# Kernel optimization log

Measured on AMD Instinct MI355X. Metric: run time of the kernel, lower is better.

Reference implementation:

```python
import jax, jax.numpy as jnp
import numpy as np
from jax import lax

B, D, H, W = 2, 96, 96, 96
K = 3          # static upper bound on connected components (setup builds exactly 3 blobs)
CC_ITERS = 48  # >= max component diameter under 26-connectivity label propagation
V = D * H * W
BIGI = jnp.int32(V)  # sentinel label for background


def _make_target():
    # 3 well-separated spherical lesions per volume -> exactly K connected components
    centers = [(20, 20, 20), (70, 30, 60), (40, 75, 75)]
    r2 = 9 ** 2
    zz, yy, xx = np.meshgrid(np.arange(D), np.arange(H), np.arange(W), indexing='ij')
    vol = np.zeros((D, H, W), np.float32)
    for cz, cy, cx in centers:
        vol[(zz - cz) ** 2 + (yy - cy) ** 2 + (xx - cx) ** 2 <= r2] = 1.0
    return jnp.asarray(np.stack([vol, np.roll(vol, 5, axis=2)])[:, None])  # [B,1,D,H,W]


def setup_inputs() -> dict:
    key = jax.random.key(0)
    pred = jax.random.normal(key, (B, 1, D, H, W), jnp.float32)
    return {"pred": pred, "target": _make_target()}


def _connected_components(mask):
    # 26-connectivity labeling (matches skimage/cucim default for 3D).
    # Label = min flat raster index in each component, so ascending-sorted labels
    # reproduce cucim's scan-order labels 1..N (needed for tie-breaking parity).
    lab = jnp.where(mask, jnp.arange(V, dtype=jnp.int32).reshape(mask.shape), BIGI)
    for _ in range(CC_ITERS):  # fixed unroll; components have diameter << CC_ITERS
        nb = lax.reduce_window(lab, BIGI, lax.min, (3, 3, 3), (1, 1, 1), 'SAME')
        lab = jnp.where(mask, nb, BIGI)
    return lab


def _edt1d(f):
    # exact 1D squared-distance lower envelope: d[i] = min_j f[j] + (i-j)^2
    n = f.shape[-1]
    i = jnp.arange(n, dtype=jnp.float32)
    sq = (i[:, None] - i[None, :]) ** 2  # [n_out, n_in]
    return jnp.min(f[..., None, :] + sq, axis=-1)


def _squared_edt(seed):
    # exact squared Euclidean distance-to-seed via 3 separable passes
    f = jnp.where(seed, jnp.float32(0), jnp.float32(1e12))
    for ax in range(3):
        f = jnp.moveaxis(_edt1d(jnp.moveaxis(f, ax, -1)), -1, ax)
    return f


def _forward(pred, target):
    p = jax.nn.sigmoid(pred)[:, 0]  # dim==5 -> sigmoid; squeeze channel -> [B,D,H,W]
    g = target[:, 0]

    def labels(gt):
        lab = _connected_components(gt > 0.5)
        ul = jnp.unique(lab, size=K + 1, fill_value=BIGI)[:K]  # ascending = scan order
        return lab, ul

    lab, ul = jax.vmap(labels)(g)                 # lab [B,D,H,W], ul [B,K]
    valid = (ul < BIGI).astype(p.dtype)           # [B,K]
    seeds = lab[:, None] == ul[:, :, None, None, None]  # [B,K,D,H,W] bool
    # serial map over (B*K) regions keeps the [D,H,W,n] EDT intermediate to one at a time
    dists = lax.map(_squared_edt, seeds.reshape(B * K, D, H, W)).reshape(B, K, D, H, W)
    # squared vs sqrt distance: same ordering AND same ties as torch's strict '<' update;
    rmap = jnp.argmin(dists, axis=1)              # Voronoi region map [B,D,H,W]

    oh = jax.nn.one_hot(rmap, K, dtype=p.dtype)   # [B,D,H,W,K]
    inter = jnp.einsum('bdhw,bdhwk->bk', p * g, oh)
    psum = jnp.einsum('bdhw,bdhwk->bk', p, oh)
    gsum = jnp.einsum('bdhw,bdhwk->bk', g, oh)
    dice = 2.0 * inter / (psum + gsum + 1e-8)
    cnt = jnp.sum(valid, axis=1)
    mean_dice = jnp.sum(dice * valid, axis=1) / jnp.maximum(cnt, 1.0)
    loss = jnp.where(cnt > 0, 1.0 - mean_dice, 1.0)  # num_features==0 -> loss 1.0
    return jnp.mean(loss)


def reference(pred, target):
    return _forward(pred, target)
```

## Files before the change

### kernel.cpp

```cpp
#include <hip/hip_runtime.h>
#include <math.h>

#define SLICE 9216
#define VOL 884736
#define NB 2
#define KK 3
#define BIGI VOL
#define BIGP 0x3FFFFFFC
#define BIGPF 1.0e9f
#define CC_SWEEPS 4
#define NYC 4
#define NZC 4
#define NPART (NB*96*NZC)
#define MAXROW 64
#define MAXNZ 64
#define YSTR (MAXNZ*96)

#define OFF_ACT   (NB*VOL*4)
#define OFF_DISTC (2*NB*VOL*4)
#define DISTC_BYTES (NB*96*MAXNZ*96*4)
#define OFF_SMALL (OFF_DISTC + DISTC_BYTES)
#define OFF_ZMASK (OFF_SMALL + 64)
#define OFF_ROOTS (OFF_SMALL + 128)
#define OFF_MASK  (OFF_SMALL + 1024)
#define MASK_ULL  (NB*KK*96*96*2)
#define OFF_PART  (OFF_MASK + MASK_ULL*8)
#define OFF_M8    (OFF_PART + NPART*9*4)

__global__ void k_init(const float4* __restrict__ tgt4, int* __restrict__ lab,
                       int* __restrict__ act, int* __restrict__ small,
                       unsigned long long* __restrict__ masks,
                       unsigned char* __restrict__ m8) {
  int q = blockIdx.x * 256 + threadIdx.x;
  if (q < MASK_ULL) masks[q] = 0;
  if (q >= NB * VOL / 4) return;
  float4 tv = tgt4[q];
  int base = q * 4;
  int bo = (base >= VOL) ? VOL : 0;
  int4 lv;
  lv.x = (tv.x > 0.5f) ? base - bo     : BIGI;
  lv.y = (tv.y > 0.5f) ? base - bo + 1 : BIGI;
  lv.z = (tv.z > 0.5f) ? base - bo + 2 : BIGI;
  lv.w = (tv.w > 0.5f) ? base - bo + 3 : BIGI;
  ((int4*)lab)[q] = lv;
  unsigned char mb = (tv.x > 0.5f ? 1 : 0) | (tv.y > 0.5f ? 2 : 0) |
                     (tv.z > 0.5f ? 4 : 0) | (tv.w > 0.5f ? 8 : 0);
  m8[q] = mb;
  int cnt = (lv.x != BIGI) + (lv.y != BIGI) + (lv.z != BIGI) + (lv.w != BIGI);
  if (cnt) {
    int pos = atomicAdd(&small[0], cnt);
    if (lv.x != BIGI) act[pos++] = base;
    if (lv.y != BIGI) act[pos++] = base + 1;
    if (lv.z != BIGI) act[pos++] = base + 2;
    if (lv.w != BIGI) act[pos]   = base + 3;
  }
}

__global__ void k_prop(int* __restrict__ lab, const int* __restrict__ act,
                       int* __restrict__ small, int record,
                       int* __restrict__ roots) {
  int n = small[0];
  for (int i = blockIdx.x * blockDim.x + threadIdx.x; i < n;
       i += gridDim.x * blockDim.x) {
    int idx = act[i];
    int bo = (idx >= VOL) ? VOL : 0;
    int v = idx - bo;
    int z = v / SLICE;
    int rem = v - z * SLICE;
    int y = rem / 96;
    int x = rem - y * 96;
    int* L = lab + bo;
    int z0 = z > 0 ? z - 1 : 0, z1 = z < 95 ? z + 1 : 95;
    int y0 = y > 0 ? y - 1 : 0, y1 = y < 95 ? y + 1 : 95;
    int x0 = x > 0 ? x - 1 : 0, x1 = x < 95 ? x + 1 : 95;
    int m = BIGI;
    for (int zz = z0; zz <= z1; zz++)
      for (int yy = y0; yy <= y1; yy++) {
        const int* row = L + zz * SLICE + yy * 96;
        for (int xx = x0; xx <= x1; xx++) m = min(m, row[xx]);
      }
    int m2 = L[m];
    int m3 = L[m2];
    int m4 = L[m3];
    lab[idx] = m4;
    if (record && m4 == v) {
      int b = bo ? 1 : 0;
      int pos = atomicAdd(&small[1 + b], 1);
      if (pos < 64) roots[b * 64 + pos] = v;
    }
  }
}

__global__ void k_seeds(const int* __restrict__ lab, const int* __restrict__ act,
                        const int* __restrict__ small, const int* __restrict__ roots,
                        unsigned long long* __restrict__ masks,
                        unsigned long long* __restrict__ zmg) {
  __shared__ int s_roots[128];
  __shared__ int s_ul[NB][KK];
  __shared__ unsigned long long zm[NB * 2];
  int t = threadIdx.x;
  if (t < 128) {
    int b = t >> 6, j = t & 63;
    int nr = small[1 + b]; if (nr > 64) nr = 64;
    s_roots[t] = (j < nr) ? roots[t] : 0x7fffffff;
  }
  if (t < NB * KK) s_ul[t / KK][t % KK] = -2;
  if (t < NB * 2) zm[t] = 0;
  __syncthreads();
  if (t < 128) {
    int r = s_roots[t];
    if (r != 0x7fffffff) {
      int b = t >> 6;
      int rank = 0;
      #pragma unroll
      for (int j = 0; j < 64; j++)
        rank += (s_roots[(b << 6) + j] < r) ? 1 : 0;
      if (rank < KK) s_ul[b][rank] = r;
    }
  }
  __syncthreads();
  int n = small[0];
  for (int i = blockIdx.x * 256 + t; i < n; i += gridDim.x * 256) {
    int idx = act[i];
    int b = (idx >= VOL) ? 1 : 0;
    int v = idx - (b ? VOL : 0);
    const int* L = lab + (b ? VOL : 0);
    int lv = L[v];
    int nx = L[lv];
    while (nx != lv) { lv = nx; nx = L[lv]; }
    int k = (lv == s_ul[b][0]) ? 0 : (lv == s_ul[b][1]) ? 1
          : (lv == s_ul[b][2]) ? 2 : -1;
    if (k >= 0) {
      int z = v / SLICE;
      int rem = v - z * SLICE;
      int y = rem / 96;
      int x = rem - y * 96;
      unsigned long long* M =
          masks + (((size_t)(b * KK + k) * 96 + z) * 96 + y) * 2;
      if (x < 64) atomicOr(&M[0], 1ull << x);
      else        atomicOr(&M[1], 1ull << (x - 64));
      if (z < 64) atomicOr(&zm[b * 2],     1ull << z);
      else        atomicOr(&zm[b * 2 + 1], 1ull << (z - 64));
    }
  }
  __syncthreads();
  if (t < NB * 2 && zm[t]) atomicOr(&zmg[t], zm[t]);
}

__device__ __forceinline__ int row_dist(unsigned long long lo,
                                        unsigned long long hi, int x) {
  int dr, dlft;
  {
    unsigned long long rl, rh;
    if (x == 0)      { rl = lo; rh = hi; }
    else if (x < 64) { rl = (lo >> x) | (hi << (64 - x)); rh = hi >> x; }
    else             { rl = hi >> (x - 64); rh = 0; }
    dr = rl ? (__ffsll(rl) - 1) : (rh ? (63 + __ffsll(rh)) : 1000);
  }
  {
    unsigned long long ll, lh;
    if (x >= 64) { ll = lo; lh = hi & ((2ull << (x - 64)) - 1); }
    else         { ll = lo & ((2ull << x) - 1); lh = 0; }
    dlft = lh ? (x - 127 + __clzll(lh))
              : (ll ? (x - 63 + __clzll(ll)) : 1000);
  }
  return min(dr, dlft);
}

__global__ __launch_bounds__(256) void k_edt_xy(const unsigned long long* __restrict__ masks,
                                                const unsigned long long* __restrict__ zmg,
                                                float* __restrict__ distC) {
  int blk = blockIdx.x;
  int b = blk / (MAXNZ * NYC);
  int rem = blk - b * MAXNZ * NYC;
  int jj = rem / NYC;
  int yc = rem - jj * NYC;
  unsigned long long zlo = zmg[b * 2], zhi = zmg[b * 2 + 1];
  int nlo = __popcll(zlo);
  int nz = nlo + __popcll(zhi);
  if (jj >= nz) return;
  int z;
  if (jj < nlo) {
    unsigned long long w = zlo;
    for (int i = 0; i < jj; i++) w &= w - 1;
    z = __ffsll(w) - 1;
  } else {
    unsigned long long w = zhi;
    int r2 = jj - nlo;
    for (int i = 0; i < r2; i++) w &= w - 1;
    z = 64 + __ffsll(w) - 1;
  }
  __shared__ unsigned long long sM[KK * 192];
  __shared__ float pl[MAXROW * 96];
  __shared__ unsigned char vrow[96];
  __shared__ int s_n;
  int t = threadIdx.x;
  if (t == 0) s_n = 0;
  for (int i = t; i < KK * 192; i += 256) {
    int k = i / 192, r = i - k * 192;
    sM[i] = masks[((size_t)(b * KK + k) * 96 + z) * 192 + r];
  }
  __syncthreads();
  if (t < 96) {
    unsigned long long any = sM[t * 2] | sM[t * 2 + 1] | sM[192 + t * 2] |
                             sM[193 + t * 2] | sM[384 + t * 2] | sM[385 + t * 2];
    if (any) {
      int pos = atomicAdd(&s_n, 1);
      if (pos < MAXROW) vrow[pos] = (unsigned char)t;
    }
  }
  __syncthreads();
  int n = s_n; if (n > MAXROW) n = MAXROW;
  for (int i = t; i < n * 96; i += 256) {
    int j2 = i / 96, x = i - j2 * 96;
    int y = vrow[j2];
    int best = BIGP;
    #pragma unroll
    for (int k = 0; k < KK; k++) {
      unsigned long long lo = sM[k * 192 + y * 2];
      unsigned long long hi = sM[k * 192 + y * 2 + 1];
      if (lo | hi) {
        int d = row_dist(lo, hi, x);
        best = min(best, ((d * d) << 2) | k);
      }
    }
    pl[j2 * 96 + x] = (best == BIGP) ? BIGPF : (float)best;
  }
  __syncthreads();
  for (int tt = t; tt < 288; tt += 256) {
    int x = tt % 96;
    int yg = tt / 96;
    int yy0 = yc * 24 + yg * 8;
    float acc[8];
    #pragma unroll
    for (int i2 = 0; i2 < 8; i2++) acc[i2] = BIGPF;
    for (int j2 = 0; j2 < n; j2++) {
      int j = vrow[j2];
      float f = pl[j2 * 96 + x];
      float d0 = (float)(yy0 - j);
      #pragma unroll
      for (int i2 = 0; i2 < 8; i2++) {
        float dy = d0 + (float)i2;
        acc[i2] = fminf(acc[i2], __builtin_fmaf(4.f * dy, dy, f));
      }
    }
    float* DA = distC + (size_t)b * 96 * YSTR + jj * 96 + x;
    #pragma unroll
    for (int i2 = 0; i2 < 8; i2++)
      DA[(yy0 + i2) * YSTR] = acc[i2];
  }
}

__global__ __launch_bounds__(256) void k_z_fuse(const float* __restrict__ distC,
                                                const unsigned long long* __restrict__ zmg,
                                                const float* __restrict__ pred,
                                                const unsigned char* __restrict__ m8,
                                                float* __restrict__ part,
                                                int* __restrict__ small,
                                                float* __restrict__ out) {
  int blk = blockIdx.x;
  int b = blk / (96 * NZC);
  int rem = blk - b * 96 * NZC;
  int y = rem / NZC;
  int zc = rem - y * NZC;
  __shared__ float g[MAXNZ * 96];
  __shared__ unsigned char zl[96];
  __shared__ int s_last;
  __shared__ float wsum[4][9];
  int t = threadIdx.x;
  if (t == 0) s_last = 0;
  unsigned long long zlo = zmg[b * 2], zhi = zmg[b * 2 + 1];
  int nz = __popcll(zlo) + __popcll(zhi);
  if (nz > MAXNZ) nz = MAXNZ;
  if (t < 96) {
    int set = (t < 64) ? (int)((zlo >> t) & 1) : (int)((zhi >> (t - 64)) & 1);
    if (set) {
      int jj;
      if (t < 64) jj = __popcll(zlo & ((t ? (1ull << t) : 1ull) - 1ull));
      else        jj = __popcll(zlo) + __popcll(zhi & ((1ull << (t - 64)) - 1ull));
      if (jj < MAXNZ) zl[jj] = (unsigned char)t;
    }
  }
  {
    const float4* src4 = (const float4*)(distC + (size_t)(b * 96 + y) * YSTR);
    float4* g4 = (float4*)g;
    int n4 = nz * 24;
    for (int i = t; i < n4; i += 256) g4[i] = src4[i];
  }
  __syncthreads();
  const float* P = pred + (size_t)b * VOL + y * 96;
  const unsigned char* M8 = m8 + ((size_t)b * VOL + y * 96) / 4;
  float a0 = 0.f, a1 = 0.f, a2 = 0.f, a3 = 0.f, a4 = 0.f,
        a5 = 0.f, a6 = 0.f, a7 = 0.f, a8 = 0.f;
  for (int tt = t; tt < 288; tt += 256) {
    int xg = tt % 24;
    int zg = tt / 24;
    int x4 = xg * 4;
    int zz0 = zc * 24 + zg * 2;
    float pv[8];
    *(float4*)&pv[0] = *(const float4*)&P[zz0 * SLICE + x4];
    *(float4*)&pv[4] = *(const float4*)&P[(zz0 + 1) * SLICE + x4];
    unsigned int mb0 = M8[(zz0 * SLICE + x4) >> 2];
    unsigned int mb1 = M8[((zz0 + 1) * SLICE + x4) >> 2];
    float acc[8];
    #pragma unroll
    for (int i2 = 0; i2 < 8; i2++) acc[i2] = BIGPF;
    for (int jj = 0; jj < nz; jj++) {
      float4 gq = *(const float4*)&g[jj * 96 + x4];
      float d0 = (float)(zz0 - (int)zl[jj]);
      float d1 = d0 + 1.f;
      acc[0] = fminf(acc[0], __builtin_fmaf(4.f * d0, d0, gq.x));
      acc[1] = fminf(acc[1], __builtin_fmaf(4.f * d0, d0, gq.y));
      acc[2] = fminf(acc[2], __builtin_fmaf(4.f * d0, d0, gq.z));
      acc[3] = fminf(acc[3], __builtin_fmaf(4.f * d0, d0, gq.w));
      acc[4] = fminf(acc[4], __builtin_fmaf(4.f * d1, d1, gq.x));
      acc[5] = fminf(acc[5], __builtin_fmaf(4.f * d1, d1, gq.y));
      acc[6] = fminf(acc[6], __builtin_fmaf(4.f * d1, d1, gq.z));
      acc[7] = fminf(acc[7], __builtin_fmaf(4.f * d1, d1, gq.w));
    }
    #pragma unroll
    for (int i2 = 0; i2 < 8; i2++) {
      int iz = i2 >> 2, j = i2 & 3;
      float p = __builtin_amdgcn_rcpf(1.f + __expf(-pv[iz * 4 + j]));
      float gg = (float)(((iz ? mb1 : mb0) >> j) & 1);
      int kk = ((int)acc[iz * 4 + j]) & 3;
      float pg = p * gg;
      a0 += (kk == 0) ? pg : 0.f;
      a1 += (kk == 1) ? pg : 0.f;
      a2 += (kk == 2) ? pg : 0.f;
      a3 += (kk == 0) ? p : 0.f;
      a4 += (kk == 1) ? p : 0.f;
      a5 += (kk == 2) ? p : 0.f;
      a6 += (kk == 0) ? gg : 0.f;
      a7 += (kk == 1) ? gg : 0.f;
      a8 += (kk == 2) ? gg : 0.f;
    }
  }
  float s[9] = {a0, a1, a2, a3, a4, a5, a6, a7, a8};
  #pragma unroll
  for (int off = 32; off > 0; off >>= 1)
    #pragma unroll
    for (int q = 0; q < 9; q++) s[q] += __shfl_down(s[q], off);
  int wave = t >> 6, lane = t & 63;
  if (lane == 0) {
    #pragma unroll
    for (int q = 0; q < 9; q++) wsum[wave][q] = s[q];
  }
  __syncthreads();
  if (t < 9)
    part[blk * 9 + t] = wsum[0][t] + wsum[1][t] + wsum[2][t] + wsum[3][t];
  __syncthreads();
  if (t == 0) {
    __threadfence();
    int c = atomicAdd(&small[3], 1);
    s_last = (c == NPART - 1) ? 1 : 0;
  }
  __syncthreads();
  if (!s_last) return;
  __threadfence();
  float a[18];
  #pragma unroll
  for (int q = 0; q < 18; q++) a[q] = 0.f;
  for (int r = t; r < NPART; r += 256) {
    int bb = r / (96 * NZC);
    #pragma unroll
    for (int q = 0; q < 9; q++) a[bb * 9 + q] += part[r * 9 + q];
  }
  #pragma unroll
  for (int off = 32; off > 0; off >>= 1)
    #pragma unroll
    for (int q = 0; q < 18; q++) a[q] += __shfl_down(a[q], off);
  __shared__ float fs[4][18];
  if (lane == 0) {
    #pragma unroll
    for (int q = 0; q < 18; q++) fs[wave][q] = a[q];
  }
  __syncthreads();
  if (t == 0) {
    float tot[18];
    #pragma unroll
    for (int q = 0; q < 18; q++)
      tot[q] = fs[0][q] + fs[1][q] + fs[2][q] + fs[3][q];
    float loss = 0.f;
    for (int bb = 0; bb < NB; bb++) {
      int cnt = small[1 + bb];
      if (cnt > KK) cnt = KK;
      float ds = 0.f;
      for (int k = 0; k < cnt; k++) {
        float inter = tot[bb * 9 + k];
        float ps = tot[bb * 9 + 3 + k];
        float gs = tot[bb * 9 + 6 + k];
        ds += 2.f * inter / (ps + gs + 1e-8f);
      }
      float mean = ds / fmaxf((float)cnt, 1.f);
      loss += (cnt > 0) ? (1.f - mean) : 1.f;
    }
    out[0] = loss * 0.5f;
  }
}

extern "C" void kernel_launch(void* const* d_in, const int* in_sizes, int n_in,
                              void* d_out, int out_size, void* d_ws, size_t ws_size,
                              hipStream_t stream) {
  const float* pred = (const float*)d_in[0];
  const float* tgt  = (const float*)d_in[1];
  float* out = (float*)d_out;

  char* ws = (char*)d_ws;
  int* lab   = (int*)(ws);
  int* act   = (int*)(ws + OFF_ACT);
  float* distC = (float*)(ws + OFF_DISTC);
  int* small = (int*)(ws + OFF_SMALL);
  unsigned long long* zmg = (unsigned long long*)(ws + OFF_ZMASK);
  int* roots = (int*)(ws + OFF_ROOTS);
  unsigned long long* masks = (unsigned long long*)(ws + OFF_MASK);
  float* part = (float*)(ws + OFF_PART);
  unsigned char* m8 = (unsigned char*)(ws + OFF_M8);

  hipMemsetAsync(ws + OFF_SMALL, 0, 128, stream);
  k_init<<<(NB * VOL / 4 + 255) / 256, 256, 0, stream>>>(
      (const float4*)tgt, lab, act, small, masks, m8);
  for (int it = 0; it < CC_SWEEPS; it++)
    k_prop<<<96, 256, 0, stream>>>(lab, act, small, it == CC_SWEEPS - 1 ? 1 : 0, roots);
  k_seeds<<<96, 256, 0, stream>>>(lab, act, small, roots, masks, zmg);
  k_edt_xy<<<NB * MAXNZ * NYC, 256, 0, stream>>>(masks, zmg, distC);
  k_z_fuse<<<NB * 96 * NZC, 256, 0, stream>>>(distC, zmg, pred, m8, part, small, out);
}
```

Baseline: 154.4 us.

## Split z range into eight chunks per row, one z-slice per thread

Measured after the change: 171.5 us. 11.0% more time.

```diff
diff --git a/kernel.cpp b/kernel.cpp
--- a/kernel.cpp
+++ b/kernel.cpp
@@ -10,7 +10,7 @@
 #define BIGPF 1.0e9f
 #define CC_SWEEPS 4
 #define NYC 4
-#define NZC 4
+#define NZC 8
 #define NPART (NB*96*NZC)
 #define MAXROW 64
 #define MAXNZ 64
@@ -294,36 +294,28 @@
         a5 = 0.f, a6 = 0.f, a7 = 0.f, a8 = 0.f;
   for (int tt = t; tt < 288; tt += 256) {
     int xg = tt % 24;
-    int zg = tt / 24;
+    int zz = zc * 12 + tt / 24;
     int x4 = xg * 4;
-    int zz0 = zc * 24 + zg * 2;
-    float pv[8];
-    *(float4*)&pv[0] = *(const float4*)&P[zz0 * SLICE + x4];
-    *(float4*)&pv[4] = *(const float4*)&P[(zz0 + 1) * SLICE + x4];
-    unsigned int mb0 = M8[(zz0 * SLICE + x4) >> 2];
-    unsigned int mb1 = M8[((zz0 + 1) * SLICE + x4) >> 2];
-    float acc[8];
-    #pragma unroll
-    for (int i2 = 0; i2 < 8; i2++) acc[i2] = BIGPF;
+    float4 pq = *(const float4*)&P[zz * SLICE + x4];
+    unsigned int mb = M8[(zz * SLICE + x4) >> 2];
+    float acc[4];
+    #pragma unroll
+    for (int i2 = 0; i2 < 4; i2++) acc[i2] = BIGPF;
     for (int jj = 0; jj < nz; jj++) {
       float4 gq = *(const float4*)&g[jj * 96 + x4];
-      float d0 = (float)(zz0 - (int)zl[jj]);
-      float d1 = d0 + 1.f;
-      acc[0] = fminf(acc[0], __builtin_fmaf(4.f * d0, d0, gq.x));
-      acc[1] = fminf(acc[1], __builtin_fmaf(4.f * d0, d0, gq.y));
-      acc[2] = fminf(acc[2], __builtin_fmaf(4.f * d0, d0, gq.z));
-      acc[3] = fminf(acc[3], __builtin_fmaf(4.f * d0, d0, gq.w));
-      acc[4] = fminf(acc[4], __builtin_fmaf(4.f * d1, d1, gq.x));
-      acc[5] = fminf(acc[5], __builtin_fmaf(4.f * d1, d1, gq.y));
-      acc[6] = fminf(acc[6], __builtin_fmaf(4.f * d1, d1, gq.z));
-      acc[7] = fminf(acc[7], __builtin_fmaf(4.f * d1, d1, gq.w));
-    }
-    #pragma unroll
-    for (int i2 = 0; i2 < 8; i2++) {
-      int iz = i2 >> 2, j = i2 & 3;
-      float p = __builtin_amdgcn_rcpf(1.f + __expf(-pv[iz * 4 + j]));
-      float gg = (float)(((iz ? mb1 : mb0) >> j) & 1);
-      int kk = ((int)acc[iz * 4 + j]) & 3;
+      float d0 = (float)(zz - (int)zl[jj]);
+      float dd = 4.f * d0 * d0;
+      acc[0] = fminf(acc[0], gq.x + dd);
+      acc[1] = fminf(acc[1], gq.y + dd);
+      acc[2] = fminf(acc[2], gq.z + dd);
+      acc[3] = fminf(acc[3], gq.w + dd);
+    }
+    float pv[4] = {pq.x, pq.y, pq.z, pq.w};
+    #pragma unroll
+    for (int j = 0; j < 4; j++) {
+      float p = __builtin_amdgcn_rcpf(1.f + __expf(-pv[j]));
+      float gg = (float)((mb >> j) & 1);
+      int kk = ((int)acc[j]) & 3;
       float pg = p * gg;
       a0 += (kk == 0) ? pg : 0.f;
       a1 += (kk == 1) ? pg : 0.f;
```
